# Kernel optimization log

Hardware: AMD Instinct MI355X
Metric: run time of the kernel (lower is better)

## Reference

```python
import jax, jax.numpy as jnp
import numpy as np

L = 1024            # sequence length (env states fed as inputs_embeds)
D_IN = 4            # raw state dim
D_MODEL = 768       # mamba hidden size (mamba-130m-class backbone)
N_LAYERS = 24
D_INNER = 1536      # expand(2) * d_model
D_STATE = 16
D_CONV = 4
DT_RANK = 48        # d_model // 16
EPS = 1e-5


def setup_inputs():
    key = jax.random.key(0)
    ks = jax.random.split(key, 8)
    s = 0.02
    def nrm(k, sh, sc=s):
        return jax.random.normal(k, sh, dtype=jnp.float32) * sc
    # dt bias init: softplus^{-1}(0.01), as in Mamba reference init
    dt_bias = jnp.log(jnp.expm1(jnp.full((N_LAYERS, D_INNER), 0.01, dtype=jnp.float32)))
    # S4D-real init: A_nd = n+1
    A_log = jnp.log(jnp.broadcast_to(jnp.arange(1, D_STATE + 1, dtype=jnp.float32),
                                     (N_LAYERS, D_INNER, D_STATE)))
    return {
        "x": jax.random.normal(ks[0], (L, D_IN), dtype=jnp.float32),
        "w_enc": nrm(ks[1], (D_IN, D_MODEL), 0.5),
        "b_enc": jnp.zeros((D_MODEL,), jnp.float32),
        "norm_w": jnp.ones((N_LAYERS, D_MODEL), jnp.float32),
        "in_proj_w": nrm(ks[2], (N_LAYERS, D_MODEL, 2 * D_INNER)),
        "conv_w": nrm(ks[3], (N_LAYERS, D_INNER, D_CONV), 0.1),
        "conv_b": jnp.zeros((N_LAYERS, D_INNER), jnp.float32),
        "x_proj_w": nrm(ks[4], (N_LAYERS, D_INNER, DT_RANK + 2 * D_STATE)),
        "dt_proj_w": nrm(ks[5], (N_LAYERS, DT_RANK, D_INNER)),
        "dt_proj_b": dt_bias,
        "A_log": A_log,
        "D_skip": jnp.ones((N_LAYERS, D_INNER), jnp.float32),
        "out_proj_w": nrm(ks[6], (N_LAYERS, D_INNER, D_MODEL)),
        "norm_f_w": jnp.ones((D_MODEL,), jnp.float32),
        "fc_w": nrm(ks[7], (D_MODEL, 2), 0.05),
        "fc_b": jnp.zeros((2,), jnp.float32),
    }


def _rmsnorm(x, w):
    return x * jax.lax.rsqrt(jnp.mean(x * x, axis=-1, keepdims=True) + EPS) * w


def _mamba_block(u, p):
    # u: [L, D_MODEL]; pre-norm residual Mamba block
    norm_w, in_w, cw, cb, xp_w, dt_w, dt_b, A_log, D_skip, out_w = p
    h = _rmsnorm(u, norm_w)
    xz = h @ in_w                                   # [L, 2*D_INNER]
    xpart, z = jnp.split(xz, 2, axis=-1)
    # causal depthwise conv1d (kernel D_CONV, left-padded)
    xc = jax.lax.conv_general_dilated(
        xpart.T[None], cw[:, None, :], (1,), [(D_CONV - 1, 0)],
        feature_group_count=D_INNER)[0].T + cb      # [L, D_INNER]
    xc = jax.nn.silu(xc)
    dbl = xc @ xp_w                                 # [L, DT_RANK + 2*D_STATE]
    dt = jax.nn.softplus(dbl[:, :DT_RANK] @ dt_w + dt_b)   # [L, D_INNER]
    B = dbl[:, DT_RANK:DT_RANK + D_STATE]           # [L, D_STATE]
    C = dbl[:, DT_RANK + D_STATE:]                  # [L, D_STATE]
    A = -jnp.exp(A_log)                             # [D_INNER, D_STATE]
    dA = jnp.exp(dt[:, :, None] * A[None])          # [L, D_INNER, D_STATE]
    dBx = dt[:, :, None] * B[:, None, :] * xc[:, :, None]

    def step(hst, t):
        dA_t, dBx_t, C_t = t
        hst = dA_t * hst + dBx_t                    # [D_INNER, D_STATE]
        return hst, hst @ C_t                       # y_t: [D_INNER]

    _, ys = jax.lax.scan(step, jnp.zeros((D_INNER, D_STATE), xc.dtype), (dA, dBx, C))
    y = (ys + D_skip * xc) * jax.nn.silu(z)
    return u + y @ out_w


def reference(x, w_enc, b_enc, norm_w, in_proj_w, conv_w, conv_b, x_proj_w,
              dt_proj_w, dt_proj_b, A_log, D_skip, out_proj_w, norm_f_w, fc_w, fc_b):
    u = x @ w_enc + b_enc                           # state_encoder: [L, D_MODEL]
    params = (norm_w, in_proj_w, conv_w, conv_b, x_proj_w, dt_proj_w,
              dt_proj_b, A_log, D_skip, out_proj_w)
    block = jax.checkpoint(_mamba_block)
    u, _ = jax.lax.scan(lambda c, p: (block(c, p), None), u, params)
    u = _rmsnorm(u, norm_f_w)
    return (u[-1] @ fc_w + fc_b)[None, :]           # logits [1, 2]
```

## Files before the change

### kernel.cpp

```cpp
#include <hip/hip_runtime.h>
#include <hip/hip_bf16.h>

#define L_SEQ 1024
#define D_MODEL 768
#define D_INNER 1536
#define D_STATE 16
#define DT_RANK 48
#define N_LAYERS 24
#define NCHUNK 16
#define CS (L_SEQ / NCHUNK)
#define KSPLIT_OUT 4
#define DTN 128

typedef __attribute__((ext_vector_type(8))) short short8;
typedef __attribute__((ext_vector_type(4))) float f32x4;

__device__ inline ushort rtn1(float v) {
  unsigned b = __float_as_uint(v);
  return (ushort)((b + 0x7FFF + ((b >> 16) & 1)) >> 16);
}

__device__ inline void gload16(const void* g, void* l) {
  __builtin_amdgcn_global_load_lds(
      (const __attribute__((address_space(1))) void*)g,
      (__attribute__((address_space(3))) void*)l, 16, 0, 0);
}

__global__ __launch_bounds__(256) void tsplit_k(
    const float* __restrict__ in, ushort* __restrict__ hi, int K, int N,
    int Kp) {
  __shared__ float tile[64][65];
  const int l = blockIdx.z;
  const float* src = in + (size_t)l * K * N;
  ushort* dh = hi + (size_t)l * N * Kp;
  const int n0 = blockIdx.x * 64, k0 = blockIdx.y * 64;
  const int tx = threadIdx.x & 63, ty = threadIdx.x >> 6;
#pragma unroll
  for (int rr = 0; rr < 16; rr++) {
    int ky = rr * 4 + ty;
    int k = k0 + ky;
    tile[ky][tx] = (k < K) ? src[(size_t)k * N + n0 + tx] : 0.f;
  }
  __syncthreads();
  const int txk = threadIdx.x & 31;
  const int tyn = threadIdx.x >> 5;
#pragma unroll
  for (int rr = 0; rr < 8; rr++) {
    int ny = rr * 8 + tyn;
    unsigned p = (unsigned)rtn1(tile[2 * txk][ny]) |
                 ((unsigned)rtn1(tile[2 * txk + 1][ny]) << 16);
    *(unsigned*)&dh[(size_t)(n0 + ny) * Kp + k0 + 2 * txk] = p;
  }
}

__global__ __launch_bounds__(256) void gemm_bf16(
    const ushort* __restrict__ A, int lda, const ushort* __restrict__ B,
    int ldb, float* __restrict__ C, int ldc, int K) {
  __shared__ ushort lds[2][192 * 32];

  const int tid = threadIdx.x;
  const int bm = blockIdx.y * 128;
  const int bn = blockIdx.x * 64;
  const int kz0 = blockIdx.z * K;
  const int lane = tid & 63;
  const int wid = tid >> 6;
  const int wm = wid & 1, wn = wid >> 1;
  const int r = lane & 15, g = lane >> 4;
  const int segrow = lane >> 2;
  const int segch = lane & 3;

  auto stage = [&](int buf, int k0) {
#pragma unroll
    for (int i = 0; i < 3; i++) {
      int s = wid * 3 + i;
      int gr = s * 16 + segrow;
      int rt = gr & 63;
      int ch = segch ^ ((rt >> 1) & 3);
      bool isA = gr < 128;
      const ushort* src = isA ? A : B;
      int row = isA ? (bm + gr) : (bn + gr - 128);
      int ld = isA ? lda : ldb;
      gload16(src + (size_t)row * ld + k0 + ch * 8, &lds[buf][s * 512]);
    }
  };

  f32x4 acc[4][2] = {};
  const int nt = K / 32;

  stage(0, kz0);

  for (int t = 0; t < nt; t++) {
    const int cur = t & 1;
    if (t + 1 < nt) {
      stage(cur ^ 1, kz0 + (t + 1) * 32);
      asm volatile("s_waitcnt vmcnt(3)" ::: "memory");
    } else {
      asm volatile("s_waitcnt vmcnt(0)" ::: "memory");
    }
    __builtin_amdgcn_s_barrier();
    __builtin_amdgcn_sched_barrier(0);

    short8 af[4], bf[2];
#pragma unroll
    for (int m = 0; m < 4; m++) {
      int row = wm * 64 + m * 16 + r;
      int gg = g ^ ((row >> 1) & 3);
      af[m] = *reinterpret_cast<short8*>(&lds[cur][row * 32 + gg * 8]);
    }
#pragma unroll
    for (int n = 0; n < 2; n++) {
      int row = wn * 32 + n * 16 + r;
      int gg = g ^ ((row >> 1) & 3);
      bf[n] = *reinterpret_cast<short8*>(&lds[cur][(128 + row) * 32 + gg * 8]);
    }
#pragma unroll
    for (int m = 0; m < 4; m++)
#pragma unroll
      for (int n = 0; n < 2; n++)
        acc[m][n] = __builtin_amdgcn_mfma_f32_16x16x32_bf16(
            af[m], bf[n], acc[m][n], 0, 0, 0);
    __builtin_amdgcn_s_barrier();
  }

  float* Cz = C + (size_t)blockIdx.z * gridDim.y * 128 * ldc;
#pragma unroll
  for (int m = 0; m < 4; m++) {
#pragma unroll
    for (int n = 0; n < 2; n++) {
      int row0 = bm + wm * 64 + m * 16 + g * 4;
      int col = bn + wn * 32 + n * 16 + r;
#pragma unroll
      for (int j = 0; j < 4; j++)
        Cz[(size_t)(row0 + j) * ldc + col] = acc[m][n][j];
    }
  }
}

__global__ __launch_bounds__(256) void encode_k(
    const float* __restrict__ x, const float* __restrict__ w_enc,
    const float* __restrict__ b_enc, float* __restrict__ u) {
  int d = blockIdx.x * 256 + threadIdx.x;
  int t = blockIdx.y;
  const float4 xv = *(const float4*)(x + t * 4);
  float acc = b_enc[d];
  acc = fmaf(xv.x, w_enc[0 * D_MODEL + d], acc);
  acc = fmaf(xv.y, w_enc[1 * D_MODEL + d], acc);
  acc = fmaf(xv.z, w_enc[2 * D_MODEL + d], acc);
  acc = fmaf(xv.w, w_enc[3 * D_MODEL + d], acc);
  u[t * D_MODEL + d] = acc;
}

__global__ __launch_bounds__(256) void rmsnorm_b_k(
    const float* __restrict__ u, const float* __restrict__ w,
    ushort* __restrict__ hb) {
  int t = blockIdx.x;
  const float* ur = u + t * D_MODEL;
  float ss = 0.f;
  float vl[3];
#pragma unroll
  for (int p = 0; p < 3; p++) {
    int d = threadIdx.x + p * 256;
    vl[p] = ur[d];
    ss = fmaf(vl[p], vl[p], ss);
  }
#pragma unroll
  for (int o = 1; o < 64; o <<= 1) ss += __shfl_xor(ss, o);
  __shared__ float red[4];
  int wid = threadIdx.x >> 6;
  if ((threadIdx.x & 63) == 0) red[wid] = ss;
  __syncthreads();
  float rs = rsqrtf((red[0] + red[1] + red[2] + red[3]) / (float)D_MODEL +
                    1e-5f);
#pragma unroll
  for (int p = 0; p < 3; p++) {
    int d = threadIdx.x + p * 256;
    hb[t * D_MODEL + d] = rtn1(vl[p] * rs * w[d]);
  }
}

__global__ __launch_bounds__(256) void rmsnorm_add_k(
    const float* __restrict__ Po, float* __restrict__ u,
    const float* __restrict__ w, ushort* __restrict__ hb) {
  int t = blockIdx.x;
  float* ur = u + t * D_MODEL;
  float ss = 0.f;
  float vl[3];
#pragma unroll
  for (int p = 0; p < 3; p++) {
    int d = threadIdx.x + p * 256;
    float v = ur[d];
#pragma unroll
    for (int z = 0; z < KSPLIT_OUT; z++)
      v += Po[(size_t)z * L_SEQ * D_MODEL + (size_t)t * D_MODEL + d];
    ur[d] = v;
    vl[p] = v;
    ss = fmaf(v, v, ss);
  }
#pragma unroll
  for (int o = 1; o < 64; o <<= 1) ss += __shfl_xor(ss, o);
  __shared__ float red[4];
  int wid = threadIdx.x >> 6;
  if ((threadIdx.x & 63) == 0) red[wid] = ss;
  __syncthreads();
  float rs = rsqrtf((red[0] + red[1] + red[2] + red[3]) / (float)D_MODEL +
                    1e-5f);
#pragma unroll
  for (int p = 0; p < 3; p++) {
    int d = threadIdx.x + p * 256;
    hb[t * D_MODEL + d] = rtn1(vl[p] * rs * w[d]);
  }
}

#define DBL_NS 8
#define DBL_KSEG (D_INNER / DBL_NS)
__global__ __launch_bounds__(256) void gemm_dblconv_k(
    const float* __restrict__ xz, const float* __restrict__ cw,
    const float* __restrict__ cb, const float* __restrict__ B,
    float* __restrict__ P, float* __restrict__ xc) {
  __shared__ float As2[16][17];
  __shared__ float Bs2[16][80];
  const int tid = threadIdx.x;
  const int bm = blockIdx.y * 16;
  const int ks0 = blockIdx.x * DBL_KSEG;
  const int tx = tid % 16;
  const int ty = tid / 16;
  const int sm = tid / 16, sk = tid % 16;
  const int t = bm + sm;

  float4 wv;
  float cbv, xv0, xv1, xv2, xv3, bv0, bv1, bv2, bv3, bv4;
  auto issue = [&](int k0) {
    int c = k0 + sk;
    wv = *(const float4*)(cw + c * 4);
    cbv = cb[c];
    xv0 = (t >= 3) ? xz[(size_t)(t - 3) * 2 * D_INNER + c] : 0.f;
    xv1 = (t >= 2) ? xz[(size_t)(t - 2) * 2 * D_INNER + c] : 0.f;
    xv2 = (t >= 1) ? xz[(size_t)(t - 1) * 2 * D_INNER + c] : 0.f;
    xv3 = xz[(size_t)t * 2 * D_INNER + c];
    bv0 = B[(size_t)(k0 + (tid + 0) / 80) * 80 + (tid + 0) % 80];
    bv1 = B[(size_t)(k0 + (tid + 256) / 80) * 80 + (tid + 256) % 80];
    bv2 = B[(size_t)(k0 + (tid + 512) / 80) * 80 + (tid + 512) % 80];
    bv3 = B[(size_t)(k0 + (tid + 768) / 80) * 80 + (tid + 768) % 80];
    bv4 = B[(size_t)(k0 + (tid + 1024) / 80) * 80 + (tid + 1024) % 80];
  };

  float acc[5] = {0.f, 0.f, 0.f, 0.f, 0.f};

  issue(ks0);

  for (int k0 = ks0; k0 < ks0 + DBL_KSEG; k0 += 16) {
    float a = cbv;
    a = fmaf(xv0, wv.x, a);
    a = fmaf(xv1, wv.y, a);
    a = fmaf(xv2, wv.z, a);
    a = fmaf(xv3, wv.w, a);
    float v = a / (1.f + __expf(-a));
    xc[(size_t)t * D_INNER + k0 + sk] = v;
    As2[sk][sm] = v;
    Bs2[(tid + 0) / 80][(tid + 0) % 80] = bv0;
    Bs2[(tid + 256) / 80][(tid + 256) % 80] = bv1;
    Bs2[(tid + 512) / 80][(tid + 512) % 80] = bv2;
    Bs2[(tid + 768) / 80][(tid + 768) % 80] = bv3;
    Bs2[(tid + 1024) / 80][(tid + 1024) % 80] = bv4;
    if (k0 + 16 < ks0 + DBL_KSEG) issue(k0 + 16);
    asm volatile("s_waitcnt lgkmcnt(0)" ::: "memory");
    __builtin_amdgcn_s_barrier();
    __builtin_amdgcn_sched_barrier(0);
#pragma unroll
    for (int k = 0; k < 16; k++) {
      float ra = As2[k][ty];
#pragma unroll
      for (int j = 0; j < 5; j++) acc[j] = fmaf(ra, Bs2[k][tx * 5 + j], acc[j]);
    }
    __builtin_amdgcn_s_barrier();
  }

  float* p = P + ((size_t)blockIdx.x * L_SEQ + bm + ty) * 80 + tx * 5;
#pragma unroll
  for (int j = 0; j < 5; j++) p[j] = acc[j];
}

__global__ __launch_bounds__(256) void reduce_dt_k(
    const float* __restrict__ P, const float* __restrict__ dtw,
    const float* __restrict__ dtbias, float* __restrict__ dbl,
    float* __restrict__ dtb) {
  __shared__ float s_dbl[16][48];
  __shared__ float wch[48][DTN + 1];
  const int tid = threadIdx.x;
  const int cc = blockIdx.x * DTN;
  const int bm = blockIdx.y * 16;

  for (int i = tid; i < 16 * 80; i += 256) {
    int rr = i / 80, col = i % 80;
    float s = 0.f;
#pragma unroll
    for (int ks = 0; ks < DBL_NS; ks++)
      s += P[((size_t)ks * L_SEQ + bm + rr) * 80 + col];
    if (col < DT_RANK) s_dbl[rr][col] = s;
    if (blockIdx.x == 0) dbl[(size_t)(bm + rr) * 80 + col] = s;
  }
  for (int i = tid; i < DT_RANK * DTN; i += 256) {
    int j = i / DTN, c = i % DTN;
    wch[j][c] = dtw[(size_t)j * D_INNER + cc + c];
  }
  __syncthreads();

  const int row = tid >> 4, cl = tid & 15;
#pragma unroll
  for (int i = 0; i < DTN / 16; i++) {
    int c = cl + i * 16;
    float s = dtbias[cc + c];
#pragma unroll
    for (int j = 0; j < DT_RANK; j++) s = fmaf(s_dbl[row][j], wch[j][c], s);
    dtb[(size_t)(bm + row) * D_INNER + cc + c] =
        (s > 20.f) ? s : log1pf(__expf(s));
  }
}

__global__ __launch_bounds__(256) void scan1_k(
    const float* __restrict__ dt, const float* __restrict__ xc,
    const float* __restrict__ dbl, const float* __restrict__ A_log,
    float* __restrict__ Pb, float* __restrict__ Eb) {
  __shared__ float s_dt[CS][16];
  __shared__ float s_xc[CS][16];
  __shared__ float s_b[CS][16];
  const int tid = threadIdx.x;
  const int s = tid & 15;
  const int cl = tid >> 4;
  const int c0 = blockIdx.y * 16;
  const int c = c0 + cl;
  const int t0 = blockIdx.x * CS;
  const float a = -__expf(A_log[c * D_STATE + s]);

  const int lc = tid & 15, lt = tid >> 4;
#pragma unroll
  for (int p = 0; p < CS / 16; p++) {
    int t = lt + p * 16;
    size_t gt = (size_t)(t0 + t);
    s_dt[t][lc] = dt[gt * D_INNER + c0 + lc];
    s_xc[t][lc] = xc[gt * D_INNER + c0 + lc];
    s_b[t][lc] = dbl[gt * 80 + DT_RANK + lc];
  }
  __syncthreads();

  float P = 1.f, h = 0.f;
  for (int t = 0; t < CS; t++) {
    float dtv = s_dt[t][cl];
    float dA = __expf(dtv * a);
    P *= dA;
    h = fmaf(dA, h, dtv * s_b[t][s] * s_xc[t][cl]);
  }
  int idx = blockIdx.x * (D_INNER * D_STATE) + c0 * D_STATE + tid;
  Pb[idx] = P;
  Eb[idx] = h;
}

__global__ __launch_bounds__(256) void scan3_k(
    const float* __restrict__ dt, const float* __restrict__ xc,
    const float* __restrict__ dbl, const float* __restrict__ xz,
    const float* __restrict__ A_log, const float* __restrict__ D_skip,
    const float* __restrict__ Pb, const float* __restrict__ Eb,
    ushort* __restrict__ yb16) {
  __shared__ float s_dt[CS][16];
  __shared__ float s_xc[CS][16];
  __shared__ float s_z[CS][16];
  __shared__ float s_bc[CS][32];

  const int tid = threadIdx.x;
  const int s = tid & 15;
  const int cl = tid >> 4;
  const int c0 = blockIdx.y * 16;
  const int c = c0 + cl;
  const int t0 = blockIdx.x * CS;

  const float a = -__expf(A_log[c * D_STATE + s]);
  const float Dv = D_skip[c];

  const int lc = tid & 15, lt = tid >> 4;
  const int bj = tid & 31, bt = tid >> 5;
#pragma unroll
  for (int p = 0; p < CS / 16; p++) {
    int t = lt + p * 16;
    size_t gt = (size_t)(t0 + t);
    s_dt[t][lc] = dt[gt * D_INNER + c0 + lc];
    s_xc[t][lc] = xc[gt * D_INNER + c0 + lc];
    s_z[t][lc] = xz[gt * 2 * D_INNER + D_INNER + c0 + lc];
  }
#pragma unroll
  for (int p = 0; p < CS / 8; p++) {
    int t = bt + p * 8;
    s_bc[t][bj] = dbl[(size_t)(t0 + t) * 80 + DT_RANK + bj];
  }

  float hst = 0.f;
  {
    const int nj = blockIdx.x;
    const int base = c0 * D_STATE + tid;
    float pj[NCHUNK - 1], ej[NCHUNK - 1];
#pragma unroll
    for (int jj = 0; jj < NCHUNK - 1; jj++) {
      if (jj < nj) {
        int o = jj * (D_INNER * D_STATE) + base;
        pj[jj] = Pb[o];
        ej[jj] = Eb[o];
      }
    }
#pragma unroll
    for (int jj = 0; jj < NCHUNK - 1; jj++)
      if (jj < nj) hst = fmaf(pj[jj], hst, ej[jj]);
  }
  __syncthreads();

  for (int t = 0; t < CS; t++) {
    float dtv = s_dt[t][cl];
    float xv = s_xc[t][cl];
    float Bv = s_bc[t][s];
    float Cv = s_bc[t][16 + s];
    float dA = __expf(dtv * a);
    hst = fmaf(dA, hst, dtv * Bv * xv);
    float p2 = hst * Cv;
    p2 += __shfl_xor(p2, 1);
    p2 += __shfl_xor(p2, 2);
    p2 += __shfl_xor(p2, 4);
    p2 += __shfl_xor(p2, 8);
    if (s == 0) {
      float zv = s_z[t][cl];
      float sz = zv / (1.f + __expf(-zv));
      yb16[(size_t)(t0 + t) * D_INNER + c] = rtn1((p2 + Dv * xv) * sz);
    }
  }
}

__global__ __launch_bounds__(256) void final_k(
    const float* __restrict__ u, const float* __restrict__ Po,
    const float* __restrict__ nfw, const float* __restrict__ fcw,
    const float* __restrict__ fcb, float* __restrict__ out) {
  const float* ur = u + (size_t)(L_SEQ - 1) * D_MODEL;
  float ss = 0.f;
  float vl[3];
#pragma unroll
  for (int p = 0; p < 3; p++) {
    int d = threadIdx.x + p * 256;
    float v = ur[d];
#pragma unroll
    for (int z = 0; z < KSPLIT_OUT; z++)
      v += Po[(size_t)z * L_SEQ * D_MODEL + (size_t)(L_SEQ - 1) * D_MODEL + d];
    vl[p] = v;
    ss = fmaf(v, v, ss);
  }
#pragma unroll
  for (int o = 1; o < 64; o <<= 1) ss += __shfl_xor(ss, o);
  __shared__ float red[4];
  int wid = threadIdx.x >> 6;
  if ((threadIdx.x & 63) == 0) red[wid] = ss;
  __syncthreads();
  float rs = rsqrtf((red[0] + red[1] + red[2] + red[3]) / (float)D_MODEL +
                    1e-5f);
  float a0 = 0.f, a1 = 0.f;
#pragma unroll
  for (int p = 0; p < 3; p++) {
    int d = threadIdx.x + p * 256;
    float hn = vl[p] * rs * nfw[d];
    a0 = fmaf(hn, fcw[d * 2 + 0], a0);
    a1 = fmaf(hn, fcw[d * 2 + 1], a1);
  }
#pragma unroll
  for (int o = 1; o < 64; o <<= 1) {
    a0 += __shfl_xor(a0, o);
    a1 += __shfl_xor(a1, o);
  }
  __shared__ float r0[4], r1[4];
  if ((threadIdx.x & 63) == 0) {
    r0[wid] = a0;
    r1[wid] = a1;
  }
  __syncthreads();
  if (threadIdx.x == 0) out[0] = r0[0] + r0[1] + r0[2] + r0[3] + fcb[0];
  if (threadIdx.x == 1) out[1] = r1[0] + r1[1] + r1[2] + r1[3] + fcb[1];
}

extern "C" void kernel_launch(void* const* d_in, const int* in_sizes, int n_in,
                              void* d_out, int out_size, void* d_ws,
                              size_t ws_size, hipStream_t stream) {
  const float* x      = (const float*)d_in[0];
  const float* w_enc  = (const float*)d_in[1];
  const float* b_enc  = (const float*)d_in[2];
  const float* norm_w = (const float*)d_in[3];
  const float* in_w   = (const float*)d_in[4];
  const float* conv_w = (const float*)d_in[5];
  const float* conv_b = (const float*)d_in[6];
  const float* xp_w   = (const float*)d_in[7];
  const float* dt_w   = (const float*)d_in[8];
  const float* dt_b   = (const float*)d_in[9];
  const float* A_log  = (const float*)d_in[10];
  const float* D_skip = (const float*)d_in[11];
  const float* out_w  = (const float*)d_in[12];
  const float* nf_w   = (const float*)d_in[13];
  const float* fc_w   = (const float*)d_in[14];
  const float* fc_b   = (const float*)d_in[15];
  float* out = (float*)d_out;

  float* u   = (float*)d_ws;
  float* xzb = u   + (size_t)L_SEQ * D_MODEL;
  float* xcb = xzb + (size_t)L_SEQ * 2 * D_INNER;
  float* dbl = xcb + (size_t)L_SEQ * D_INNER;
  float* dtb = dbl + (size_t)L_SEQ * 80;
  float* yb  = dtb + (size_t)L_SEQ * D_INNER;
  float* Po  = yb  + (size_t)L_SEQ * 80 * DBL_NS;
  float* Pb  = Po  + (size_t)KSPLIT_OUT * L_SEQ * D_MODEL;
  float* Eb  = Pb  + (size_t)NCHUNK * D_INNER * D_STATE;
  float* fend = Eb + (size_t)NCHUNK * D_INNER * D_STATE;

  ushort* hb   = (ushort*)fend;
  ushort* yb16 = hb + (size_t)L_SEQ * D_MODEL;
  ushort* wxT  = yb16 + (size_t)L_SEQ * D_INNER;
  ushort* woT  = wxT + (size_t)N_LAYERS * 2 * D_INNER * D_MODEL;

  tsplit_k<<<dim3(2 * D_INNER / 64, D_MODEL / 64, N_LAYERS), 256, 0, stream>>>(
      in_w, wxT, D_MODEL, 2 * D_INNER, D_MODEL);
  tsplit_k<<<dim3(D_MODEL / 64, D_INNER / 64, N_LAYERS), 256, 0, stream>>>(
      out_w, woT, D_INNER, D_MODEL, D_INNER);

  encode_k<<<dim3(3, L_SEQ), 256, 0, stream>>>(x, w_enc, b_enc, u);

  for (int l = 0; l < N_LAYERS; l++) {
    const float* cw_l    = conv_w + (size_t)l * D_INNER * 4;
    const float* cb_l    = conv_b + (size_t)l * D_INNER;
    const float* xp_w_l  = xp_w  + (size_t)l * D_INNER * 80;
    const float* dt_w_l  = dt_w  + (size_t)l * DT_RANK * D_INNER;
    const float* dt_b_l  = dt_b  + (size_t)l * D_INNER;
    const float* A_log_l = A_log + (size_t)l * D_INNER * D_STATE;
    const float* D_l     = D_skip + (size_t)l * D_INNER;
    const ushort* wxT_l = wxT + (size_t)l * 2 * D_INNER * D_MODEL;
    const ushort* woT_l = woT + (size_t)l * D_MODEL * D_INNER;

    if (l == 0) {
      rmsnorm_b_k<<<L_SEQ, 256, 0, stream>>>(
          u, norm_w + (size_t)l * D_MODEL, hb);
    } else {
      rmsnorm_add_k<<<L_SEQ, 256, 0, stream>>>(
          Po, u, norm_w + (size_t)l * D_MODEL, hb);
    }
    gemm_bf16<<<dim3(2 * D_INNER / 64, L_SEQ / 128), 256, 0, stream>>>(
        hb, D_MODEL, wxT_l, D_MODEL, xzb, 2 * D_INNER, D_MODEL);
    gemm_dblconv_k<<<dim3(DBL_NS, L_SEQ / 16), 256, 0, stream>>>(
        xzb, cw_l, cb_l, xp_w_l, yb, xcb);
    reduce_dt_k<<<dim3(D_INNER / DTN, L_SEQ / 16), 256, 0, stream>>>(
        yb, dt_w_l, dt_b_l, dbl, dtb);
    scan1_k<<<dim3(NCHUNK, D_INNER / 16), 256, 0, stream>>>(
        dtb, xcb, dbl, A_log_l, Pb, Eb);
    scan3_k<<<dim3(NCHUNK, D_INNER / 16), 256, 0, stream>>>(
        dtb, xcb, dbl, xzb, A_log_l, D_l, Pb, Eb, yb16);
    gemm_bf16<<<dim3(D_MODEL / 64, L_SEQ / 128, KSPLIT_OUT), 256, 0,
                stream>>>(yb16, D_INNER, woT_l, D_INNER, Po, D_MODEL,
                          D_INNER / KSPLIT_OUT);
  }

  final_k<<<1, 256, 0, stream>>>(u, Po, nf_w, fc_w, fc_b, out);
}
```

Baseline: 2.704 ms.

## Fuse split-K reduction and dt projection into the first chunked scan kernel

Merges reduce_dt_k and scan1_k into one kernel tiled by (time chunk, 16 channels). Each block reduces the split-K partials for its 64 timesteps, computes softplus(dt) into shared memory and runs the chunk-local scan directly, so one launch goes away and the dt round-trip through global memory before scan1 is avoided. In exchange, every one of the 96 channel blocks per chunk repeats the partial-sum reduction (DBL_NS reads per element), which adds redundant global traffic.

```diff
diff --git a/kernel.cpp b/kernel.cpp
--- a/kernel.cpp
+++ b/kernel.cpp
@@ -10,7 +10,6 @@
 #define NCHUNK 16
 #define CS (L_SEQ / NCHUNK)
 #define KSPLIT_OUT 4
-#define DTN 128
 
 typedef __attribute__((ext_vector_type(8))) short short8;
 typedef __attribute__((ext_vector_type(4))) float f32x4;
@@ -280,78 +279,75 @@
   for (int j = 0; j < 5; j++) p[j] = acc[j];
 }
 
-__global__ __launch_bounds__(256) void reduce_dt_k(
+__global__ __launch_bounds__(256) void rds1_k(
     const float* __restrict__ P, const float* __restrict__ dtw,
-    const float* __restrict__ dtbias, float* __restrict__ dbl,
-    float* __restrict__ dtb) {
-  __shared__ float s_dbl[16][48];
-  __shared__ float wch[48][DTN + 1];
+    const float* __restrict__ dtbias, const float* __restrict__ xc,
+    const float* __restrict__ A_log, float* __restrict__ dbl,
+    float* __restrict__ dtb, float* __restrict__ Pb,
+    float* __restrict__ Eb) {
+  __shared__ float s_dbl[CS][49];
+  __shared__ float s_bc[CS][32];
+  __shared__ float wch[DT_RANK][16];
+  __shared__ float s_dt[CS][16];
+  __shared__ float s_xc[CS][16];
+
   const int tid = threadIdx.x;
-  const int cc = blockIdx.x * DTN;
-  const int bm = blockIdx.y * 16;
-
-  for (int i = tid; i < 16 * 80; i += 256) {
+  const int t0 = blockIdx.x * CS;
+  const int c0 = blockIdx.y * 16;
+
+  for (int i = tid; i < CS * 80; i += 256) {
     int rr = i / 80, col = i % 80;
     float s = 0.f;
 #pragma unroll
     for (int ks = 0; ks < DBL_NS; ks++)
-      s += P[((size_t)ks * L_SEQ + bm + rr) * 80 + col];
-    if (col < DT_RANK) s_dbl[rr][col] = s;
-    if (blockIdx.x == 0) dbl[(size_t)(bm + rr) * 80 + col] = s;
-  }
-  for (int i = tid; i < DT_RANK * DTN; i += 256) {
-    int j = i / DTN, c = i % DTN;
-    wch[j][c] = dtw[(size_t)j * D_INNER + cc + c];
-  }
-  __syncthreads();
-
-  const int row = tid >> 4, cl = tid & 15;
-#pragma unroll
-  for (int i = 0; i < DTN / 16; i++) {
-    int c = cl + i * 16;
-    float s = dtbias[cc + c];
-#pragma unroll
-    for (int j = 0; j < DT_RANK; j++) s = fmaf(s_dbl[row][j], wch[j][c], s);
-    dtb[(size_t)(bm + row) * D_INNER + cc + c] =
-        (s > 20.f) ? s : log1pf(__expf(s));
-  }
-}
-
-__global__ __launch_bounds__(256) void scan1_k(
-    const float* __restrict__ dt, const float* __restrict__ xc,
-    const float* __restrict__ dbl, const float* __restrict__ A_log,
-    float* __restrict__ Pb, float* __restrict__ Eb) {
-  __shared__ float s_dt[CS][16];
-  __shared__ float s_xc[CS][16];
-  __shared__ float s_b[CS][16];
-  const int tid = threadIdx.x;
+      s += P[((size_t)ks * L_SEQ + t0 + rr) * 80 + col];
+    if (col < DT_RANK)
+      s_dbl[rr][col] = s;
+    else
+      s_bc[rr][col - DT_RANK] = s;
+    if (blockIdx.y == 0 && col >= DT_RANK)
+      dbl[(size_t)(t0 + rr) * 80 + col] = s;
+  }
+  for (int i = tid; i < DT_RANK * 16; i += 256)
+    wch[i >> 4][i & 15] = dtw[(size_t)(i >> 4) * D_INNER + c0 + (i & 15)];
+  {
+    const int lc = tid & 15, lt = tid >> 4;
+#pragma unroll
+    for (int p = 0; p < CS / 16; p++) {
+      int t = lt + p * 16;
+      s_xc[t][lc] = xc[(size_t)(t0 + t) * D_INNER + c0 + lc];
+    }
+  }
+  __syncthreads();
+
+  {
+    const int row4 = tid >> 4, cl = tid & 15;
+    float bias = dtbias[c0 + cl];
+#pragma unroll
+    for (int i = 0; i < CS / 16; i++) {
+      int r = row4 + i * 16;
+      float s = bias;
+#pragma unroll
+      for (int j = 0; j < DT_RANK; j++) s = fmaf(s_dbl[r][j], wch[j][cl], s);
+      float sp = (s > 20.f) ? s : log1pf(__expf(s));
+      s_dt[r][cl] = sp;
+      dtb[(size_t)(t0 + r) * D_INNER + c0 + cl] = sp;
+    }
+  }
+  __syncthreads();
+
   const int s = tid & 15;
   const int cl = tid >> 4;
-  const int c0 = blockIdx.y * 16;
-  const int c = c0 + cl;
-  const int t0 = blockIdx.x * CS;
-  const float a = -__expf(A_log[c * D_STATE + s]);
-
-  const int lc = tid & 15, lt = tid >> 4;
-#pragma unroll
-  for (int p = 0; p < CS / 16; p++) {
-    int t = lt + p * 16;
-    size_t gt = (size_t)(t0 + t);
-    s_dt[t][lc] = dt[gt * D_INNER + c0 + lc];
-    s_xc[t][lc] = xc[gt * D_INNER + c0 + lc];
-    s_b[t][lc] = dbl[gt * 80 + DT_RANK + lc];
-  }
-  __syncthreads();
-
-  float P = 1.f, h = 0.f;
+  const float a = -__expf(A_log[(c0 + cl) * D_STATE + s]);
+  float Pp = 1.f, h = 0.f;
   for (int t = 0; t < CS; t++) {
     float dtv = s_dt[t][cl];
     float dA = __expf(dtv * a);
-    P *= dA;
-    h = fmaf(dA, h, dtv * s_b[t][s] * s_xc[t][cl]);
+    Pp *= dA;
+    h = fmaf(dA, h, dtv * s_bc[t][s] * s_xc[t][cl]);
   }
   int idx = blockIdx.x * (D_INNER * D_STATE) + c0 * D_STATE + tid;
-  Pb[idx] = P;
+  Pb[idx] = Pp;
   Eb[idx] = h;
 }
 
@@ -545,10 +541,8 @@
         hb, D_MODEL, wxT_l, D_MODEL, xzb, 2 * D_INNER, D_MODEL);
     gemm_dblconv_k<<<dim3(DBL_NS, L_SEQ / 16), 256, 0, stream>>>(
         xzb, cw_l, cb_l, xp_w_l, yb, xcb);
-    reduce_dt_k<<<dim3(D_INNER / DTN, L_SEQ / 16), 256, 0, stream>>>(
-        yb, dt_w_l, dt_b_l, dbl, dtb);
-    scan1_k<<<dim3(NCHUNK, D_INNER / 16), 256, 0, stream>>>(
-        dtb, xcb, dbl, A_log_l, Pb, Eb);
+    rds1_k<<<dim3(NCHUNK, D_INNER / 16), 256, 0, stream>>>(
+        yb, dt_w_l, dt_b_l, xcb, A_log_l, dbl, dtb, Pb, Eb);
     scan3_k<<<dim3(NCHUNK, D_INNER / 16), 256, 0, stream>>>(
         dtb, xcb, dbl, xzb, A_log_l, D_l, Pb, Eb, yb16);
     gemm_bf16<<<dim3(D_MODEL / 64, L_SEQ / 128, KSPLIT_OUT), 256, 0,
```

Result: slower. 2.916 ms (+7.8%).
